# Kernel optimization log

Measured on AMD Instinct MI355X. Metric: run time of the kernel, lower is better.

The kernel has to match this reference:

```python
import jax, jax.numpy as jnp
import numpy as np

B, S, D, H = 4, 2048, 512, 8
PHD = D // H  # per-head dim = 64
EPS = 1e-09


def setup_inputs() -> dict:
    k = jax.random.key(0)
    ks = jax.random.split(k, 12)
    sd = 1.0 / np.sqrt(D)
    inp = {
        "key": jax.random.normal(ks[0], (B, S, D), jnp.float32),
        "value": jax.random.normal(ks[1], (B, S, D), jnp.float32),
        "query": jax.random.normal(ks[2], (B, S, D), jnp.float32),
        "Wq": jax.random.normal(ks[3], (D, D), jnp.float32) * sd,
        "bq": jnp.zeros((D,), jnp.float32),
        "Wk": jax.random.normal(ks[4], (D, D), jnp.float32) * sd,
        "bk": jnp.zeros((D,), jnp.float32),
        "Wv": jax.random.normal(ks[5], (D, D), jnp.float32) * sd,
        "bv": jnp.zeros((D,), jnp.float32),
        "Wo": jax.random.normal(ks[6], (D, D), jnp.float32) * sd,
        "bo": jnp.zeros((D,), jnp.float32),
        "w_a": jnp.ones((D,), jnp.float32),
        "w_b": jnp.zeros((D,), jnp.float32),
    }
    return inp


def reference(key, value, query, Wq, bq, Wk, bk, Wv, bv, Wo, bo, w_a, w_b):
    residual = query
    q = query @ Wq.T + bq  # [B,S,D]
    kk = key @ Wk.T + bk
    v = value @ Wv.T + bv
    # faithful to torch .view(B*H, -1, PHD) on contiguous [B,S,D] (row-major)
    q = q.reshape(B * H, -1, PHD)
    kk = kk.reshape(B * H, -1, PHD)
    v = v.reshape(B * H, -1, PHD)
    scale = D ** (-0.5)  # note: model_dim, not per-head dim (as in source)
    attn = jnp.einsum("bqd,bkd->bqk", q, kk) * scale  # [B*H, L, L]
    attn = jax.nn.softmax(attn, axis=-1)
    context = jnp.einsum("bqk,bkd->bqd", attn, v)
    context = context.reshape(B, -1, D)
    out = context @ Wo.T + bo
    x = residual + out
    # torch LayerNorm variant: unbiased std, eps added to std
    mean = x.mean(axis=-1, keepdims=True)
    std = jnp.std(x, axis=-1, keepdims=True, ddof=1)
    output = w_a * (x - mean) / (std + EPS) + w_b
    return (output, attn)
```

## Files before the change

### kernel.cpp

```cpp
#include <hip/hip_runtime.h>
#include <hip/hip_bf16.h>
#include <cstdint>
#include <cstddef>

typedef __bf16 bf16_t;
typedef __bf16 bf16x4 __attribute__((ext_vector_type(4)));
typedef __bf16 bf16x8 __attribute__((ext_vector_type(8)));
typedef float f32x4 __attribute__((ext_vector_type(4)));

#define MFMA16(a,b,c) __builtin_amdgcn_mfma_f32_16x16x32_bf16((a),(b),(c),0,0,0)


template<bool XF32>
__device__ __forceinline__ void gemm_core(const void* __restrict__ Xp,
                                          const float* __restrict__ W,
                                          const float* __restrict__ bias,
                                          const float* __restrict__ residual,
                                          bf16_t* __restrict__ out)
{
    __shared__ __align__(16) bf16_t As[128*32];
    __shared__ __align__(16) bf16_t Bs[128*32];
    const int tid  = threadIdx.x;
    const int lane = tid & 63;
    const int w    = tid >> 6;
    const int wm   = (w & 1) * 64;
    const int wn   = (w >> 1) * 64;
    const int bm   = blockIdx.y * 128;
    const int bn   = blockIdx.x * 128;
    const int fr   = lane & 15;
    const int fq8  = (lane >> 4) * 8;

    f32x4 acc[4][4];
#pragma unroll
    for (int i = 0; i < 4; i++)
#pragma unroll
        for (int j = 0; j < 4; j++)
            acc[i][j] = (f32x4){0.f, 0.f, 0.f, 0.f};

    const int srow = tid >> 2;
    const int scol = (tid & 3) * 8;

    for (int k0 = 0; k0 < 512; k0 += 32) {
        __syncthreads();
        if constexpr (XF32) {
            const float* X = (const float*)Xp;
#pragma unroll
            for (int c = 0; c < 4; c++) {
                const int chunk = c*256 + tid;
                const int row = chunk >> 3;
                const int cc  = (chunk & 7) * 4;
                f32x4 xv = *(const f32x4*)(X + (size_t)(bm + row)*512 + k0 + cc);
                bf16x4 b = {(bf16_t)xv[0], (bf16_t)xv[1], (bf16_t)xv[2], (bf16_t)xv[3]};
                *(bf16x4*)(&As[row*32 + cc]) = b;
            }
        } else {
            const bf16_t* X = (const bf16_t*)Xp;
            *(bf16x8*)(&As[srow*32 + scol])      = *(const bf16x8*)(X + (size_t)(bm + srow)*512      + k0 + scol);
            *(bf16x8*)(&As[(64+srow)*32 + scol]) = *(const bf16x8*)(X + (size_t)(bm + 64 + srow)*512 + k0 + scol);
        }
#pragma unroll
        for (int c = 0; c < 4; c++) {
            const int chunk = c*256 + tid;
            const int row = chunk >> 3;
            const int cc  = (chunk & 7) * 4;
            f32x4 wv = *(const f32x4*)(W + (size_t)(bn + row)*512 + k0 + cc);
            bf16x4 b = {(bf16_t)wv[0], (bf16_t)wv[1], (bf16_t)wv[2], (bf16_t)wv[3]};
            *(bf16x4*)(&Bs[row*32 + cc]) = b;
        }
        __syncthreads();
        bf16x8 af[4], bfv[4];
#pragma unroll
        for (int i = 0; i < 4; i++) {
            af[i]  = *(const bf16x8*)(&As[(wm + i*16 + fr)*32 + fq8]);
            bfv[i] = *(const bf16x8*)(&Bs[(wn + i*16 + fr)*32 + fq8]);
        }
#pragma unroll
        for (int i = 0; i < 4; i++)
#pragma unroll
            for (int j = 0; j < 4; j++)
                acc[i][j] = MFMA16(af[i], bfv[j], acc[i][j]);
    }

    const int q4 = (lane >> 4) * 4;
#pragma unroll
    for (int j = 0; j < 4; j++) {
        const int col = bn + wn + j*16 + fr;
        const float bcol = bias[col];
#pragma unroll
        for (int i = 0; i < 4; i++) {
#pragma unroll
            for (int r = 0; r < 4; r++) {
                const int row = bm + wm + i*16 + q4 + r;
                float v = acc[i][j][r] + bcol;
                if (residual) v += residual[(size_t)row*512 + col];
                out[(size_t)row*512 + col] = (bf16_t)v;
            }
        }
    }
}

__global__ __launch_bounds__(256) void gemm_qkv_kernel(
    const float* __restrict__ Xq, const float* __restrict__ Xk, const float* __restrict__ Xv,
    const float* __restrict__ Wq, const float* __restrict__ Wk, const float* __restrict__ Wv,
    const float* __restrict__ bq, const float* __restrict__ bk, const float* __restrict__ bv,
    bf16_t* __restrict__ Oq, bf16_t* __restrict__ Ok, bf16_t* __restrict__ Ov)
{
    const int z = blockIdx.z;
    const float* X    = (z == 0) ? Xq : (z == 1) ? Xk : Xv;
    const float* W    = (z == 0) ? Wq : (z == 1) ? Wk : Wv;
    const float* bias = (z == 0) ? bq : (z == 1) ? bk : bv;
    bf16_t* out       = (z == 0) ? Oq : (z == 1) ? Ok : Ov;
    gemm_core<true>(X, W, bias, nullptr, out);
}

__global__ __launch_bounds__(256) void gemm_o_kernel(
    const bf16_t* __restrict__ ctx, const float* __restrict__ Wo,
    const float* __restrict__ bo, const float* __restrict__ residual,
    bf16_t* __restrict__ xout)
{
    gemm_core<false>(ctx, Wo, bo, residual, xout);
}

__global__ __launch_bounds__(256) void transpose_v_kernel(const bf16_t* __restrict__ v,
                                                          bf16_t* __restrict__ vt)
{
    __shared__ bf16_t tile[64*72];
    const int g  = blockIdx.y;
    const int t0 = blockIdx.x * 64;
    const int tid = threadIdx.x;
    const size_t gbase = (size_t)g * 131072;
#pragma unroll
    for (int c = 0; c < 2; c++) {
        const int chunk = c*256 + tid;
        const int row = chunk >> 3;
        const int cc  = (chunk & 7) * 8;
        *(bf16x8*)(&tile[row*72 + cc]) = *(const bf16x8*)(v + gbase + (size_t)(t0 + row)*64 + cc);
    }
    __syncthreads();
#pragma unroll
    for (int c = 0; c < 2; c++) {
        const int chunk = c*256 + tid;
        const int p  = chunk >> 3;
        const int tc = (chunk & 7) * 8;
        bf16x8 vv;
#pragma unroll
        for (int i = 0; i < 8; i++) vv[i] = tile[(tc + i)*72 + p];
        *(bf16x8*)(vt + gbase + (size_t)p*2048 + t0 + tc) = vv;
    }
}

__global__ __launch_bounds__(512) void attn_kernel(
    const bf16_t* __restrict__ Q, const bf16_t* __restrict__ K,
    const bf16_t* __restrict__ VT,
    float* __restrict__ attn, bf16_t* __restrict__ ctx)
{
    __shared__ __align__(16) bf16_t kb[128*64];
    __shared__ __align__(16) bf16_t vtb[64*128];
    __shared__ __align__(16) bf16_t pb[128*128];

    const int tid  = threadIdx.x;
    const int lane = tid & 63;
    const int w    = tid >> 6;
    const int fr   = lane & 15;
    const int quad = lane >> 4;
    const int g    = blockIdx.y;
    const int qt   = blockIdx.x;
    const size_t gbase = (size_t)g * 131072;

#pragma unroll
    for (int c = 0; c < 2; c++) {
        const int chunk = c*512 + tid;
        const int row = chunk >> 3;
        const int ck  = chunk & 7;
        *(bf16x8*)(&kb[row*64 + ((ck ^ (row & 7)) << 3)]) =
            *(const bf16x8*)(Q + gbase + (size_t)(qt*128 + row)*64 + ck*8);
    }
    __syncthreads();
    bf16x8 qf[2];
#pragma unroll
    for (int ks = 0; ks < 2; ks++) {
        const int row = w*16 + fr;
        const int cs = (ks*4 + quad) ^ (fr & 7);
        qf[ks] = *(const bf16x8*)(&kb[row*64 + (cs << 3)]);
    }

    const float cfac = 0.06376904269107617f;
    float lsum[4] = {0.f, 0.f, 0.f, 0.f};

    for (int kt = 0; kt < 16; kt++) {
        __syncthreads();
#pragma unroll
        for (int c = 0; c < 2; c++) {
            const int chunk = c*512 + tid;
            const int row = chunk >> 3;
            const int ck  = chunk & 7;
            *(bf16x8*)(&kb[row*64 + ((ck ^ (row & 7)) << 3)]) =
                *(const bf16x8*)(K + gbase + (size_t)(kt*128 + row)*64 + ck*8);
        }
        __syncthreads();
#pragma unroll
        for (int n = 0; n < 8; n++) {
            const int rk = n*16 + fr;
            f32x4 s = (f32x4){0.f, 0.f, 0.f, 0.f};
#pragma unroll
            for (int ks = 0; ks < 2; ks++) {
                const int cs = (ks*4 + quad) ^ (fr & 7);
                bf16x8 bv = *(const bf16x8*)(&kb[rk*64 + (cs << 3)]);
                s = MFMA16(qf[ks], bv, s);
            }
#pragma unroll
            for (int r = 0; r < 4; r++)
                lsum[r] += exp2f(s[r] * cfac);
        }
    }

    float rinv[4];
#pragma unroll
    for (int r = 0; r < 4; r++) {
        float l = lsum[r];
        l += __shfl_xor(l, 1);
        l += __shfl_xor(l, 2);
        l += __shfl_xor(l, 4);
        l += __shfl_xor(l, 8);
        rinv[r] = 1.f / l;
    }

    f32x4 oacc[4];
#pragma unroll
    for (int i = 0; i < 4; i++) oacc[i] = (f32x4){0.f, 0.f, 0.f, 0.f};

    float* abase = attn + (size_t)g*4194304 + (size_t)(qt*128)*2048;

    for (int kt = 0; kt < 16; kt++) {
        __syncthreads();
#pragma unroll
        for (int c = 0; c < 2; c++) {
            const int chunk = c*512 + tid;
            const int row = chunk >> 3;
            const int ck  = chunk & 7;
            *(bf16x8*)(&kb[row*64 + ((ck ^ (row & 7)) << 3)]) =
                *(const bf16x8*)(K + gbase + (size_t)(kt*128 + row)*64 + ck*8);
        }
#pragma unroll
        for (int c = 0; c < 2; c++) {
            const int chunk = c*512 + tid;
            const int p  = chunk >> 4;
            const int ck = chunk & 15;
            *(bf16x8*)(&vtb[p*128 + ((ck ^ (p & 15)) << 3)]) =
                *(const bf16x8*)(VT + gbase + (size_t)p*2048 + kt*128 + ck*8);
        }
        __syncthreads();
#pragma unroll
        for (int n = 0; n < 8; n++) {
            const int rk = n*16 + fr;
            f32x4 s = (f32x4){0.f, 0.f, 0.f, 0.f};
#pragma unroll
            for (int ks = 0; ks < 2; ks++) {
                const int cs = (ks*4 + quad) ^ (fr & 7);
                bf16x8 bv = *(const bf16x8*)(&kb[rk*64 + (cs << 3)]);
                s = MFMA16(qf[ks], bv, s);
            }
#pragma unroll
            for (int r = 0; r < 4; r++) {
                const float pv = exp2f(s[r] * cfac) * rinv[r];
                const int prow = w*16 + quad*4 + r;
                const int pcol = n*16 + fr;
                pb[prow*128 + ((((pcol >> 3) ^ (prow & 15)) << 3) | (pcol & 7))] = (bf16_t)pv;
                abase[(size_t)prow*2048 + kt*128 + pcol] = pv;
            }
        }
        __syncthreads();
#pragma unroll
        for (int ks = 0; ks < 4; ks++) {
            const int prow = w*16 + fr;
            const int cs = (ks*4 + quad) ^ fr;
            bf16x8 af = *(const bf16x8*)(&pb[prow*128 + (cs << 3)]);
#pragma unroll
            for (int np = 0; np < 4; np++) {
                const int vrow = np*16 + fr;
                const int cv = (ks*4 + quad) ^ fr;
                bf16x8 bv = *(const bf16x8*)(&vtb[vrow*128 + (cv << 3)]);
                oacc[np] = MFMA16(af, bv, oacc[np]);
            }
        }
    }

    const int q4 = quad * 4;
#pragma unroll
    for (int np = 0; np < 4; np++) {
#pragma unroll
        for (int r = 0; r < 4; r++) {
            const int row = qt*128 + w*16 + q4 + r;
            const int col = np*16 + fr;
            ctx[gbase + (size_t)row*64 + col] = (bf16_t)oacc[np][r];
        }
    }
}

__global__ __launch_bounds__(256) void ln_kernel(const bf16_t* __restrict__ x,
                                                 const float* __restrict__ wa,
                                                 const float* __restrict__ wb,
                                                 float* __restrict__ out)
{
    const int tid  = threadIdx.x;
    const int lane = tid & 63;
    const int w    = tid >> 6;
    const int row  = blockIdx.x * 4 + w;

    bf16x8 xv = *(const bf16x8*)(x + (size_t)row*512 + lane*8);
    float f[8];
    float s = 0.f;
#pragma unroll
    for (int i = 0; i < 8; i++) { f[i] = (float)xv[i]; s += f[i]; }
#pragma unroll
    for (int m = 1; m < 64; m <<= 1) s += __shfl_xor(s, m);
    const float mean = s * (1.0f / 512.0f);
    float sq = 0.f;
#pragma unroll
    for (int i = 0; i < 8; i++) { const float d = f[i] - mean; sq += d*d; }
#pragma unroll
    for (int m = 1; m < 64; m <<= 1) sq += __shfl_xor(sq, m);
    const float inv = 1.0f / (sqrtf(sq * (1.0f / 511.0f)) + 1e-9f);

    f32x4 wa0 = *(const f32x4*)(wa + lane*8);
    f32x4 wa1 = *(const f32x4*)(wa + lane*8 + 4);
    f32x4 wb0 = *(const f32x4*)(wb + lane*8);
    f32x4 wb1 = *(const f32x4*)(wb + lane*8 + 4);
    f32x4 o0, o1;
#pragma unroll
    for (int i = 0; i < 4; i++) {
        o0[i] = wa0[i] * (f[i]     - mean) * inv + wb0[i];
        o1[i] = wa1[i] * (f[i + 4] - mean) * inv + wb1[i];
    }
    *(f32x4*)(out + (size_t)row*512 + lane*8)     = o0;
    *(f32x4*)(out + (size_t)row*512 + lane*8 + 4) = o1;
}

extern "C" void kernel_launch(void* const* d_in, const int* in_sizes, int n_in,
                              void* d_out, int out_size, void* d_ws, size_t ws_size,
                              hipStream_t stream)
{
    (void)in_sizes; (void)n_in; (void)out_size; (void)ws_size;
    const float* key   = (const float*)d_in[0];
    const float* value = (const float*)d_in[1];
    const float* query = (const float*)d_in[2];
    const float* Wq = (const float*)d_in[3];
    const float* bq = (const float*)d_in[4];
    const float* Wk = (const float*)d_in[5];
    const float* bk = (const float*)d_in[6];
    const float* Wv = (const float*)d_in[7];
    const float* bv = (const float*)d_in[8];
    const float* Wo = (const float*)d_in[9];
    const float* bo = (const float*)d_in[10];
    const float* wa = (const float*)d_in[11];
    const float* wb = (const float*)d_in[12];
    float* out = (float*)d_out;

    char* ws = (char*)d_ws;
    bf16_t* qb   = (bf16_t*)(ws);
    bf16_t* kbuf = (bf16_t*)(ws + 8388608);
    bf16_t* vbuf = (bf16_t*)(ws + 16777216);
    bf16_t* vtb  = (bf16_t*)(ws + 25165824);
    bf16_t* ctx  = (bf16_t*)(ws + 33554432);
    bf16_t* xb   = (bf16_t*)(ws + 41943040);

    gemm_qkv_kernel<<<dim3(4, 64, 3), 256, 0, stream>>>(
        query, key, value, Wq, Wk, Wv, bq, bk, bv, qb, kbuf, vbuf);
    transpose_v_kernel<<<dim3(32, 32), 256, 0, stream>>>(vbuf, vtb);
    attn_kernel<<<dim3(16, 32), 512, 0, stream>>>(qb, kbuf, vtb, out + 4194304, ctx);
    gemm_o_kernel<<<dim3(4, 64), 256, 0, stream>>>(ctx, Wo, bo, query, xb);
    ln_kernel<<<2048, 256, 0, stream>>>(xb, wa, wb, out);
}
```

Measured before the change: 785.0 us.

## Prefetch K/V tiles into registers and coalesce attention-matrix stores via LDS

Both attention passes now load the next K (and V^T) tile into registers while the current tile is being computed, then write it to shared memory after the barrier. The second pass reuses the K and probability buffers, and the first pass gains a second K buffer for ping-ponging. The per-element scattered fp32 writes of the attention matrix are replaced by each wave reading its probability rows back from LDS and issuing contiguous 16-byte nontemporal stores. The stored attention values are now bf16-rounded before being widened to fp32, which slightly lowers output precision. The extra registers needed for prefetching may reduce occupancy.

```diff
diff --git a/kernel.cpp b/kernel.cpp
--- a/kernel.cpp
+++ b/kernel.cpp
@@ -154,9 +154,9 @@
     const bf16_t* __restrict__ VT,
     float* __restrict__ attn, bf16_t* __restrict__ ctx)
 {
-    __shared__ __align__(16) bf16_t kb[128*64];
-    __shared__ __align__(16) bf16_t vtb[64*128];
-    __shared__ __align__(16) bf16_t pb[128*128];
+    __shared__ __align__(16) bf16_t kb [128*64];
+    __shared__ __align__(16) bf16_t kb2[128*64];
+    __shared__ __align__(16) bf16_t pb [128*128];
 
     const int tid  = threadIdx.x;
     const int lane = tid & 63;
@@ -167,13 +167,16 @@
     const int qt   = blockIdx.x;
     const size_t gbase = (size_t)g * 131072;
 
-#pragma unroll
-    for (int c = 0; c < 2; c++) {
-        const int chunk = c*512 + tid;
-        const int row = chunk >> 3;
-        const int ck  = chunk & 7;
-        *(bf16x8*)(&kb[row*64 + ((ck ^ (row & 7)) << 3)]) =
-            *(const bf16x8*)(Q + gbase + (size_t)(qt*128 + row)*64 + ck*8);
+    const int c0 = tid;
+    const int c1 = 512 + tid;
+
+    {
+        const int r0 = c0 >> 3, k0c = c0 & 7;
+        const int r1 = c1 >> 3, k1c = c1 & 7;
+        *(bf16x8*)(&pb[r0*64 + ((k0c ^ (r0 & 7)) << 3)]) =
+            *(const bf16x8*)(Q + gbase + (size_t)(qt*128 + r0)*64 + k0c*8);
+        *(bf16x8*)(&pb[r1*64 + ((k1c ^ (r1 & 7)) << 3)]) =
+            *(const bf16x8*)(Q + gbase + (size_t)(qt*128 + r1)*64 + k1c*8);
     }
     __syncthreads();
     bf16x8 qf[2];
@@ -181,23 +184,29 @@
     for (int ks = 0; ks < 2; ks++) {
         const int row = w*16 + fr;
         const int cs = (ks*4 + quad) ^ (fr & 7);
-        qf[ks] = *(const bf16x8*)(&kb[row*64 + (cs << 3)]);
-    }
+        qf[ks] = *(const bf16x8*)(&pb[row*64 + (cs << 3)]);
+    }
+    {
+        const int r0 = c0 >> 3, k0c = c0 & 7;
+        const int r1 = c1 >> 3, k1c = c1 & 7;
+        *(bf16x8*)(&kb[r0*64 + ((k0c ^ (r0 & 7)) << 3)]) =
+            *(const bf16x8*)(K + gbase + (size_t)r0*64 + k0c*8);
+        *(bf16x8*)(&kb[r1*64 + ((k1c ^ (r1 & 7)) << 3)]) =
+            *(const bf16x8*)(K + gbase + (size_t)r1*64 + k1c*8);
+    }
+    __syncthreads();
 
     const float cfac = 0.06376904269107617f;
     float lsum[4] = {0.f, 0.f, 0.f, 0.f};
 
     for (int kt = 0; kt < 16; kt++) {
-        __syncthreads();
-#pragma unroll
-        for (int c = 0; c < 2; c++) {
-            const int chunk = c*512 + tid;
-            const int row = chunk >> 3;
-            const int ck  = chunk & 7;
-            *(bf16x8*)(&kb[row*64 + ((ck ^ (row & 7)) << 3)]) =
-                *(const bf16x8*)(K + gbase + (size_t)(kt*128 + row)*64 + ck*8);
-        }
-        __syncthreads();
+        bf16_t* cur = (kt & 1) ? kb2 : kb;
+        bf16_t* nxt = (kt & 1) ? kb  : kb2;
+        bf16x8 kr0, kr1;
+        if (kt < 15) {
+            kr0 = *(const bf16x8*)(K + gbase + (size_t)((kt+1)*128 + (c0 >> 3))*64 + (c0 & 7)*8);
+            kr1 = *(const bf16x8*)(K + gbase + (size_t)((kt+1)*128 + (c1 >> 3))*64 + (c1 & 7)*8);
+        }
 #pragma unroll
         for (int n = 0; n < 8; n++) {
             const int rk = n*16 + fr;
@@ -205,13 +214,20 @@
 #pragma unroll
             for (int ks = 0; ks < 2; ks++) {
                 const int cs = (ks*4 + quad) ^ (fr & 7);
-                bf16x8 bv = *(const bf16x8*)(&kb[rk*64 + (cs << 3)]);
+                bf16x8 bv = *(const bf16x8*)(&cur[rk*64 + (cs << 3)]);
                 s = MFMA16(qf[ks], bv, s);
             }
 #pragma unroll
             for (int r = 0; r < 4; r++)
                 lsum[r] += exp2f(s[r] * cfac);
         }
+        if (kt < 15) {
+            const int r0 = c0 >> 3, k0c = c0 & 7;
+            const int r1 = c1 >> 3, k1c = c1 & 7;
+            *(bf16x8*)(&nxt[r0*64 + ((k0c ^ (r0 & 7)) << 3)]) = kr0;
+            *(bf16x8*)(&nxt[r1*64 + ((k1c ^ (r1 & 7)) << 3)]) = kr1;
+        }
+        __syncthreads();
     }
 
     float rinv[4];
@@ -231,25 +247,30 @@
 
     float* abase = attn + (size_t)g*4194304 + (size_t)(qt*128)*2048;
 
+    {
+        const int r0 = c0 >> 3, k0c = c0 & 7;
+        const int r1 = c1 >> 3, k1c = c1 & 7;
+        *(bf16x8*)(&kb[r0*64 + ((k0c ^ (r0 & 7)) << 3)]) =
+            *(const bf16x8*)(K + gbase + (size_t)r0*64 + k0c*8);
+        *(bf16x8*)(&kb[r1*64 + ((k1c ^ (r1 & 7)) << 3)]) =
+            *(const bf16x8*)(K + gbase + (size_t)r1*64 + k1c*8);
+        const int p0 = c0 >> 4, v0c = c0 & 15;
+        const int p1 = c1 >> 4, v1c = c1 & 15;
+        *(bf16x8*)(&kb2[p0*128 + ((v0c ^ (p0 & 15)) << 3)]) =
+            *(const bf16x8*)(VT + gbase + (size_t)p0*2048 + v0c*8);
+        *(bf16x8*)(&kb2[p1*128 + ((v1c ^ (p1 & 15)) << 3)]) =
+            *(const bf16x8*)(VT + gbase + (size_t)p1*2048 + v1c*8);
+    }
+    __syncthreads();
+
     for (int kt = 0; kt < 16; kt++) {
-        __syncthreads();
-#pragma unroll
-        for (int c = 0; c < 2; c++) {
-            const int chunk = c*512 + tid;
-            const int row = chunk >> 3;
-            const int ck  = chunk & 7;
-            *(bf16x8*)(&kb[row*64 + ((ck ^ (row & 7)) << 3)]) =
-                *(const bf16x8*)(K + gbase + (size_t)(kt*128 + row)*64 + ck*8);
-        }
-#pragma unroll
-        for (int c = 0; c < 2; c++) {
-            const int chunk = c*512 + tid;
-            const int p  = chunk >> 4;
-            const int ck = chunk & 15;
-            *(bf16x8*)(&vtb[p*128 + ((ck ^ (p & 15)) << 3)]) =
-                *(const bf16x8*)(VT + gbase + (size_t)p*2048 + kt*128 + ck*8);
-        }
-        __syncthreads();
+        bf16x8 kr0, kr1, vr0, vr1;
+        if (kt < 15) {
+            kr0 = *(const bf16x8*)(K + gbase + (size_t)((kt+1)*128 + (c0 >> 3))*64 + (c0 & 7)*8);
+            kr1 = *(const bf16x8*)(K + gbase + (size_t)((kt+1)*128 + (c1 >> 3))*64 + (c1 & 7)*8);
+            vr0 = *(const bf16x8*)(VT + gbase + (size_t)(c0 >> 4)*2048 + (kt+1)*128 + (c0 & 15)*8);
+            vr1 = *(const bf16x8*)(VT + gbase + (size_t)(c1 >> 4)*2048 + (kt+1)*128 + (c1 & 15)*8);
+        }
 #pragma unroll
         for (int n = 0; n < 8; n++) {
             const int rk = n*16 + fr;
@@ -266,10 +287,20 @@
                 const int prow = w*16 + quad*4 + r;
                 const int pcol = n*16 + fr;
                 pb[prow*128 + ((((pcol >> 3) ^ (prow & 15)) << 3) | (pcol & 7))] = (bf16_t)pv;
-                abase[(size_t)prow*2048 + kt*128 + pcol] = pv;
-            }
-        }
-        __syncthreads();
+            }
+        }
+#pragma unroll
+        for (int i = 0; i < 8; i++) {
+            const int chunk = i*64 + lane;
+            const int rloc  = chunk >> 5;
+            const int c4    = chunk & 31;
+            const int prow  = w*16 + rloc;
+            const int pc8   = c4 >> 1;
+            const int half  = (c4 & 1) * 4;
+            bf16x4 pv4 = *(const bf16x4*)(&pb[prow*128 + (((pc8 ^ (prow & 15)) << 3) | half)]);
+            f32x4 o = {(float)pv4[0], (float)pv4[1], (float)pv4[2], (float)pv4[3]};
+            __builtin_nontemporal_store(o, (f32x4*)(abase + (size_t)prow*2048 + kt*128 + c4*4));
+        }
 #pragma unroll
         for (int ks = 0; ks < 4; ks++) {
             const int prow = w*16 + fr;
@@ -279,9 +310,21 @@
             for (int np = 0; np < 4; np++) {
                 const int vrow = np*16 + fr;
                 const int cv = (ks*4 + quad) ^ fr;
-                bf16x8 bv = *(const bf16x8*)(&vtb[vrow*128 + (cv << 3)]);
+                bf16x8 bv = *(const bf16x8*)(&kb2[vrow*128 + (cv << 3)]);
                 oacc[np] = MFMA16(af, bv, oacc[np]);
             }
+        }
+        __syncthreads();
+        if (kt < 15) {
+            const int r0 = c0 >> 3, k0c = c0 & 7;
+            const int r1 = c1 >> 3, k1c = c1 & 7;
+            *(bf16x8*)(&kb[r0*64 + ((k0c ^ (r0 & 7)) << 3)]) = kr0;
+            *(bf16x8*)(&kb[r1*64 + ((k1c ^ (r1 & 7)) << 3)]) = kr1;
+            const int p0 = c0 >> 4, v0c = c0 & 15;
+            const int p1 = c1 >> 4, v1c = c1 & 15;
+            *(bf16x8*)(&kb2[p0*128 + ((v0c ^ (p0 & 15)) << 3)]) = vr0;
+            *(bf16x8*)(&kb2[p1*128 + ((v1c ^ (p1 & 15)) << 3)]) = vr1;
+            __syncthreads();
         }
     }
 
```

After: 718.4 us. 1.09x faster.
